# Kernel optimization log

Measured on AMD Instinct MI355X. Metric: run time of the kernel, lower is better.

Reference implementation:

```python
import jax, jax.numpy as jnp
import numpy as np
import math

D_MODEL = 512
N_HEADS = 8
D_K = D_MODEL // N_HEADS
B, N = 2, 2048


def setup_inputs() -> dict:
    key = jax.random.key(0)
    ks = jax.random.split(key, 13)
    s = 1.0 / math.sqrt(D_MODEL)
    inp = {
        "x": jax.random.normal(ks[0], (B, N, D_MODEL), dtype=jnp.float32),
        "D": jax.random.uniform(ks[1], (B, N, N), dtype=jnp.float32),
        "A": jax.random.uniform(ks[2], (B, N, N), dtype=jnp.float32),
        "Wq": jax.random.normal(ks[3], (D_MODEL, D_MODEL), dtype=jnp.float32) * s,
        "bq": jnp.zeros((D_MODEL,), dtype=jnp.float32),
        "Wk": jax.random.normal(ks[4], (D_MODEL, D_MODEL), dtype=jnp.float32) * s,
        "bk": jnp.zeros((D_MODEL,), dtype=jnp.float32),
        "Wv": jax.random.normal(ks[5], (D_MODEL, D_MODEL), dtype=jnp.float32) * s,
        "bv": jnp.zeros((D_MODEL,), dtype=jnp.float32),
        "Wo": jax.random.normal(ks[6], (D_MODEL, D_MODEL), dtype=jnp.float32) * s,
        "bo": jnp.zeros((D_MODEL,), dtype=jnp.float32),
        # learned per-head bias scalars; init nonzero so biases matter numerically
        "w_d": jax.random.normal(ks[7], (1, N_HEADS, 1, 1), dtype=jnp.float32) * 0.1,
        "w_a": jax.random.normal(ks[8], (1, N_HEADS, 1, 1), dtype=jnp.float32) * 0.1,
    }
    return inp


def reference(x, D, A, Wq, bq, Wk, bk, Wv, bv, Wo, bo, w_d, w_a):
    b, n, _ = x.shape
    # project and split heads: (B, H, N, d_k)
    def heads(W, bias):
        return (x @ W.T + bias).reshape(b, n, N_HEADS, D_K).transpose(0, 2, 1, 3)
    q = heads(Wq, bq)
    k = heads(Wk, bk)
    v = heads(Wv, bv)
    scale = 1.0 / math.sqrt(D_K)
    # (B, H, N, N) scores with learned-scalar-weighted tree biases
    scores = jnp.einsum("bhqd,bhkd->bhqk", q, k) * scale
    scores = scores + w_d * D[:, None, :, :] + w_a * A[:, None, :, :]
    attn = jax.nn.softmax(scores, axis=-1)
    out = jnp.einsum("bhqk,bhkd->bhqd", attn, v)
    out = out.transpose(0, 2, 1, 3).reshape(b, n, D_MODEL)
    return out @ Wo.T + bo
```

## Files before the change

### kernel.cpp

```cpp
#include <hip/hip_runtime.h>
#include <hip/hip_bf16.h>
#include <math.h>

typedef unsigned short ushort_t;
typedef unsigned int   uint_t;
typedef __attribute__((ext_vector_type(8))) short  bf16x8;
typedef __attribute__((ext_vector_type(4))) float  f32x4;
typedef __attribute__((ext_vector_type(4))) int    int4v;
typedef __attribute__((ext_vector_type(2))) int    i32x2;
typedef __attribute__((ext_vector_type(4))) short  s16x4;

#define MFMA16(a, b, c) __builtin_amdgcn_mfma_f32_16x16x32_bf16((a), (b), (c), 0, 0, 0)

static constexpr int BATCH = 2;
static constexpr int SEQ   = 2048;
static constexpr int DMODEL = 512;
static constexpr int NHEADS = 8;
static constexpr int DK    = 64;
static constexpr int MROWS = BATCH * SEQ;
static constexpr int XE = MROWS * DMODEL;
static constexpr int WE = DMODEL * DMODEL;
static constexpr int NQKV = 3 * DMODEL;
static constexpr int NSPLIT = 4;
static constexpr int KB_PER = (SEQ / 64) / NSPLIT;

static constexpr float QSCALE_L2E = 0.18033688011112043f;
static constexpr float L2E = 1.4426950408889634f;

__device__ __forceinline__ ushort_t f2bf(float f) {
  unsigned int u = __builtin_bit_cast(unsigned int, f);
  u = (u + 0x7FFFu + ((u >> 16) & 1u)) >> 16;
  return (ushort_t)u;
}

__device__ __forceinline__ float fexp2(float x) {
  float r;
  asm("v_exp_f32 %0, %1" : "=v"(r) : "v"(x));
  return r;
}

__device__ __forceinline__ int cvt_pk_bf16(float a, float b) {
  int r;
  asm("v_cvt_pk_bf16_f32 %0, %1, %2" : "=v"(r) : "v"(a), "v"(b));
  return r;
}

__device__ __forceinline__ float rowmax16(float x) {
  int t;
  t = __builtin_amdgcn_mov_dpp(__builtin_bit_cast(int, x), 0xB1, 0xF, 0xF, true);
  x = fmaxf(x, __builtin_bit_cast(float, t));
  t = __builtin_amdgcn_mov_dpp(__builtin_bit_cast(int, x), 0x4E, 0xF, 0xF, true);
  x = fmaxf(x, __builtin_bit_cast(float, t));
  t = __builtin_amdgcn_mov_dpp(__builtin_bit_cast(int, x), 0x141, 0xF, 0xF, true);
  x = fmaxf(x, __builtin_bit_cast(float, t));
  t = __builtin_amdgcn_mov_dpp(__builtin_bit_cast(int, x), 0x140, 0xF, 0xF, true);
  x = fmaxf(x, __builtin_bit_cast(float, t));
  return x;
}

__device__ __forceinline__ void async16(const ushort_t* g, ushort_t* l) {
  __builtin_amdgcn_global_load_lds(
      (const __attribute__((address_space(1))) unsigned int*)g,
      (__attribute__((address_space(3))) unsigned int*)l, 16, 0, 0);
}

__global__ __launch_bounds__(256) void convert_kernel(
    const float* __restrict__ x,  const float* __restrict__ wq,
    const float* __restrict__ wk, const float* __restrict__ wv,
    const float* __restrict__ wo,
    const float* __restrict__ bq, const float* __restrict__ bk,
    const float* __restrict__ bv,
    ushort_t* __restrict__ dst, float* __restrict__ bqkv) {
  const int bid = blockIdx.x;
  if (bid == (XE + 4 * WE) / 1024) {
    for (int i = threadIdx.x; i < NQKV; i += 256) {
      bqkv[i] = (i < 512) ? bq[i] * QSCALE_L2E
              : (i < 1024) ? bk[i - 512] : bv[i - 1024];
    }
    return;
  }
  int e = (bid * 256 + threadIdx.x) * 4;
  const float* src;
  int off;
  float qs = 1.0f;
  if (e < XE)                { src = x;  off = e; }
  else if (e < XE + WE)      { src = wq; off = e - XE; qs = QSCALE_L2E; }
  else if (e < XE + 2 * WE)  { src = wk; off = e - XE - WE; }
  else if (e < XE + 3 * WE)  { src = wv; off = e - XE - 2 * WE; }
  else                       { src = wo; off = e - XE - 3 * WE; }
  float4 f = *reinterpret_cast<const float4*>(&src[off]);
  s16x4 v;
  v[0] = (short)f2bf(f.x * qs); v[1] = (short)f2bf(f.y * qs);
  v[2] = (short)f2bf(f.z * qs); v[3] = (short)f2bf(f.w * qs);
  *reinterpret_cast<s16x4*>(&dst[e]) = v;
}

__global__ __launch_bounds__(256) void pack_da_kernel(
    const float* __restrict__ Dm, const float* __restrict__ Am,
    uint_t* __restrict__ out) {
  int e = (blockIdx.x * 256 + threadIdx.x) * 4;
  float4 d = *reinterpret_cast<const float4*>(&Dm[e]);
  float4 a = *reinterpret_cast<const float4*>(&Am[e]);
  int4v v;
  v[0] = (int)((uint_t)f2bf(d.x) | ((uint_t)f2bf(a.x) << 16));
  v[1] = (int)((uint_t)f2bf(d.y) | ((uint_t)f2bf(a.y) << 16));
  v[2] = (int)((uint_t)f2bf(d.z) | ((uint_t)f2bf(a.z) << 16));
  v[3] = (int)((uint_t)f2bf(d.w) | ((uint_t)f2bf(a.w) << 16));
  *reinterpret_cast<int4v*>(&out[e]) = v;
}

template <bool F32OUT>
__global__ __launch_bounds__(256) void gemm_bt(
    const ushort_t* __restrict__ A, const ushort_t* __restrict__ Bt,
    const float* __restrict__ bias, void* __restrict__ C,
    int N, int K) {
  __shared__ ushort_t As[64][64];
  __shared__ ushort_t Bs[64][64];
  const int tid  = threadIdx.x;
  const int wave = tid >> 6, lane = tid & 63;
  const int quad = lane >> 4, l15 = lane & 15;
  const int m0 = blockIdx.y * 64, n0 = blockIdx.x * 64;

  f32x4 acc[4] = {};

  const int lrow = lane >> 3, slot = lane & 7;
  const int cswz = 8 * (slot ^ lrow);
  const ushort_t* ag = A  + (size_t)(m0 + wave * 16 + lrow) * K + cswz;
  const ushort_t* bg = Bt + (size_t)(n0 + wave * 16 + lrow) * K + cswz;
  ushort_t* la0 = &As[wave * 16][0];
  ushort_t* la1 = &As[wave * 16 + 8][0];
  ushort_t* lb0 = &Bs[wave * 16][0];
  ushort_t* lb1 = &Bs[wave * 16 + 8][0];

  const int swz = l15 & 7;

  for (int k0 = 0; k0 < K; k0 += 64) {
    __syncthreads();
    async16(ag + k0, la0);
    async16(ag + k0 + 8 * (size_t)K, la1);
    async16(bg + k0, lb0);
    async16(bg + k0 + 8 * (size_t)K, lb1);
    asm volatile("s_waitcnt vmcnt(0)" ::: "memory");
    __syncthreads();
#pragma unroll
    for (int s = 0; s < 2; s++) {
      const int acol = 8 * ((s * 4 + quad) ^ swz);
      bf16x8 af = *reinterpret_cast<const bf16x8*>(&As[wave * 16 + l15][acol]);
#pragma unroll
      for (int t = 0; t < 4; t++) {
        bf16x8 bfr = *reinterpret_cast<const bf16x8*>(&Bs[t * 16 + l15][acol]);
        acc[t] = MFMA16(af, bfr, acc[t]);
      }
    }
  }

#pragma unroll
  for (int t = 0; t < 4; t++) {
    const int col = n0 + t * 16 + l15;
    const float bv = bias[col];
#pragma unroll
    for (int rr = 0; rr < 4; rr++) {
      const int row = m0 + wave * 16 + quad * 4 + rr;
      const float v = acc[t][rr] + bv;
      if (F32OUT) reinterpret_cast<float*>(C)[(size_t)row * N + col] = v;
      else        reinterpret_cast<ushort_t*>(C)[(size_t)row * N + col] = f2bf(v);
    }
  }
}

__global__ __launch_bounds__(256) void attn_kernel(
    const ushort_t* __restrict__ QKV, const uint_t* __restrict__ DA,
    const float* __restrict__ wd, const float* __restrict__ wa,
    float* __restrict__ Opart, float* __restrict__ Mp, float* __restrict__ Lp) {
  const int qb = blockIdx.x, h = blockIdx.y;
  const int b = blockIdx.z / NSPLIT, split = blockIdx.z % NSPLIT;
  const int tid = threadIdx.x;
  const int wave = tid >> 6, lane = tid & 63;
  const int quad = lane >> 4, l15 = lane & 15;
  const int q0 = qb * 64;
  const float wdh = wd[h] * L2E, wah = wa[h] * L2E;

  __shared__ ushort_t Ks[64][64];
  __shared__ ushort_t Vts[64][64];
  __shared__ __align__(16) ushort_t Ps[4][16][72];

  const int qrow = q0 + wave * 16 + l15;
  bf16x8 qf[2];
#pragma unroll
  for (int s = 0; s < 2; s++)
    qf[s] = *reinterpret_cast<const bf16x8*>(
        &QKV[(size_t)(b * SEQ + qrow) * NQKV + h * DK + s * 32 + quad * 8]);

  bf16x8 ones;
#pragma unroll
  for (int j = 0; j < 8; j++) ones[j] = (short)0x3F80;

  float m_run[4], l_run[4];
  f32x4 o[4] = {};
#pragma unroll
  for (int rr = 0; rr < 4; rr++) { m_run[rr] = -INFINITY; l_run[rr] = 0.f; }

  const int lrow = lane >> 3, slot = lane & 7;
  const ushort_t* kg = QKV + (size_t)(b * SEQ + wave * 16 + lrow) * NQKV +
                       512 + h * DK + 8 * (slot ^ lrow);
  ushort_t* lk0 = &Ks[wave * 16][0];
  ushort_t* lk1 = &Ks[wave * 16 + 8][0];

  const int u  = tid >> 3;
  const int c7 = tid & 7;
  const int sc = c7 * 8;
  const int kv = ((u & 3) << 4) | (u >> 2);
  const ushort_t* vg = QKV + (size_t)(b * SEQ + kv) * NQKV + 1024 + h * DK + sc;
  const int col0 = (u & 7) + 8 * ((u >> 3) ^ c7);
  const int col1 = (u & 7) + 8 * (((u >> 3) + 4) ^ c7);

  const int swz = l15 & 7;

  const uint_t* dap[4];
#pragma unroll
  for (int rr = 0; rr < 4; rr++)
    dap[rr] = DA + (size_t)b * SEQ * SEQ +
              (size_t)(q0 + wave * 16 + quad * 4 + rr) * SEQ + l15;

  for (int kbi = 0; kbi < KB_PER; kbi++) {
    const int k0 = (split * KB_PER + kbi) * 64;
    __syncthreads();
    async16(kg + (size_t)k0 * NQKV, lk0);
    async16(kg + (size_t)(k0 + 8) * NQKV, lk1);
    bf16x8 v0 = *reinterpret_cast<const bf16x8*>(vg + (size_t)k0 * NQKV);
    bf16x8 v1 = *reinterpret_cast<const bf16x8*>(vg + (size_t)(k0 + 8) * NQKV);
#pragma unroll
    for (int j = 0; j < 8; j++) {
      Vts[sc + j][col0] = (ushort_t)v0[j];
      Vts[sc + j][col1] = (ushort_t)v1[j];
    }
    asm volatile("s_waitcnt vmcnt(0)" ::: "memory");
    __syncthreads();

    uint_t da[4][4];
#pragma unroll
    for (int t = 0; t < 4; t++) {
#pragma unroll
      for (int rr = 0; rr < 4; rr++) da[t][rr] = dap[rr][k0 + t * 16];
    }

    f32x4 sacc[4];
#pragma unroll
    for (int t = 0; t < 4; t++) {
      bf16x8 kf0 = *reinterpret_cast<const bf16x8*>(&Ks[t * 16 + l15][8 * (quad ^ swz)]);
      bf16x8 kf1 = *reinterpret_cast<const bf16x8*>(&Ks[t * 16 + l15][8 * ((4 + quad) ^ swz)]);
      f32x4 z = {};
      z = MFMA16(qf[0], kf0, z);
      sacc[t] = MFMA16(qf[1], kf1, z);
    }

    float sv[4][4];
    float mx[4] = {-INFINITY, -INFINITY, -INFINITY, -INFINITY};
#pragma unroll
    for (int t = 0; t < 4; t++) {
#pragma unroll
      for (int rr = 0; rr < 4; rr++) {
        const float fd = __builtin_bit_cast(float, da[t][rr] << 16);
        const float fa = __builtin_bit_cast(float, da[t][rr] & 0xFFFF0000u);
        float s = fmaf(wdh, fd, fmaf(wah, fa, sacc[t][rr]));
        sv[t][rr] = s;
        mx[rr] = fmaxf(mx[rr], s);
      }
    }
#pragma unroll
    for (int rr = 0; rr < 4; rr++) mx[rr] = rowmax16(mx[rr]);

    bool grow = false;
#pragma unroll
    for (int rr = 0; rr < 4; rr++) grow |= (mx[rr] > m_run[rr] + 11.5f);
    if (__ballot(grow)) {
      float alpha[4];
#pragma unroll
      for (int rr = 0; rr < 4; rr++) {
        const float mn = fmaxf(m_run[rr], mx[rr]);
        alpha[rr] = fexp2(m_run[rr] - mn);
        m_run[rr] = mn;
        l_run[rr] *= alpha[rr];
      }
#pragma unroll
      for (int dt = 0; dt < 4; dt++)
#pragma unroll
        for (int rr = 0; rr < 4; rr++) o[dt][rr] *= alpha[rr];
    }

#pragma unroll
    for (int rr = 0; rr < 4; rr++) {
      const float m = m_run[rr];
      i32x2 w;
      w[0] = cvt_pk_bf16(fexp2(sv[0][rr] - m), fexp2(sv[1][rr] - m));
      w[1] = cvt_pk_bf16(fexp2(sv[2][rr] - m), fexp2(sv[3][rr] - m));
      *reinterpret_cast<i32x2*>(&Ps[wave][quad * 4 + rr][l15 * 4]) = w;
    }

    asm volatile("s_waitcnt lgkmcnt(0)" ::: "memory");

    f32x4 rsacc = {};
#pragma unroll
    for (int s2 = 0; s2 < 2; s2++) {
      bf16x8 pf = *reinterpret_cast<const bf16x8*>(&Ps[wave][l15][s2 * 32 + quad * 8]);
#pragma unroll
      for (int dt = 0; dt < 4; dt++) {
        const int vrow = dt * 16 + l15;
        const int vcb = (s2 * 4 + quad) ^ (vrow >> 3);
        bf16x8 vf = *reinterpret_cast<const bf16x8*>(&Vts[vrow][vcb * 8]);
        o[dt] = MFMA16(pf, vf, o[dt]);
      }
      rsacc = MFMA16(pf, ones, rsacc);
    }
#pragma unroll
    for (int rr = 0; rr < 4; rr++) l_run[rr] += rsacc[rr];
  }

  const int pidx = (((b * NHEADS + h) * 32 + qb) * NSPLIT + split);
  float* op = Opart + (size_t)pidx * 4096;
#pragma unroll
  for (int dt = 0; dt < 4; dt++) {
#pragma unroll
    for (int rr = 0; rr < 4; rr++) {
      const int row = wave * 16 + quad * 4 + rr;
      op[row * 64 + dt * 16 + l15] = o[dt][rr];
    }
  }
  if (l15 == 0) {
#pragma unroll
    for (int rr = 0; rr < 4; rr++) {
      const int row = wave * 16 + quad * 4 + rr;
      Mp[(size_t)pidx * 64 + row] = m_run[rr];
      Lp[(size_t)pidx * 64 + row] = l_run[rr];
    }
  }
}

__global__ __launch_bounds__(256) void combine_kernel(
    const float* __restrict__ Opart, const float* __restrict__ Mp,
    const float* __restrict__ Lp, ushort_t* __restrict__ AO) {
  const int qb = blockIdx.x, h = blockIdx.y, b = blockIdx.z;
  const int tid = threadIdx.x;
  const int lane = tid & 63, wq = tid >> 6;
  const int pidx0 = ((b * NHEADS + h) * 32 + qb) * NSPLIT;

  for (int r = 0; r < 16; r++) {
    const int q = wq * 16 + r;
    float m[NSPLIT], l[NSPLIT];
    float M = -INFINITY;
#pragma unroll
    for (int s = 0; s < NSPLIT; s++) {
      m[s] = Mp[(size_t)(pidx0 + s) * 64 + q];
      l[s] = Lp[(size_t)(pidx0 + s) * 64 + q];
      M = fmaxf(M, m[s]);
    }
    float L = 0.f, acc = 0.f;
#pragma unroll
    for (int s = 0; s < NSPLIT; s++) {
      const float w = fexp2(m[s] - M);
      L += l[s] * w;
      acc += Opart[(size_t)(pidx0 + s) * 4096 + q * 64 + lane] * w;
    }
    const int row = b * SEQ + qb * 64 + q;
    AO[(size_t)row * DMODEL + h * DK + lane] = f2bf(acc / L);
  }
}

extern "C" void kernel_launch(void* const* d_in, const int* in_sizes, int n_in,
                              void* d_out, int out_size, void* d_ws, size_t ws_size,
                              hipStream_t stream) {
  const float* x  = (const float*)d_in[0];
  const float* Dm = (const float*)d_in[1];
  const float* Am = (const float*)d_in[2];
  const float* Wq = (const float*)d_in[3];
  const float* bq = (const float*)d_in[4];
  const float* Wk = (const float*)d_in[5];
  const float* bk = (const float*)d_in[6];
  const float* Wv = (const float*)d_in[7];
  const float* bv = (const float*)d_in[8];
  const float* Wo = (const float*)d_in[9];
  const float* bo = (const float*)d_in[10];
  const float* wd = (const float*)d_in[11];
  const float* wa = (const float*)d_in[12];

  char* ws = (char*)d_ws;
  size_t off = 0;
  ushort_t* xb    = (ushort_t*)(ws + off); off += (size_t)XE * 2;
  ushort_t* wqkvb = (ushort_t*)(ws + off); off += (size_t)3 * WE * 2;
  ushort_t* wob   = (ushort_t*)(ws + off); off += (size_t)WE * 2;
  ushort_t* QKVb  = (ushort_t*)(ws + off); off += (size_t)MROWS * NQKV * 2;
  ushort_t* AO    = (ushort_t*)(ws + off); off += (size_t)XE * 2;
  float*    bqkv  = (float*)(ws + off);    off += (size_t)NQKV * 4;
  off = (off + 255) & ~(size_t)255;
  uint_t*   DAb   = (uint_t*)(ws + off);   off += (size_t)BATCH * SEQ * SEQ * 4;
  float*    Opart = (float*)(ws + off);    off += (size_t)512 * NSPLIT * 4096 * 4;
  float*    Mpart = (float*)(ws + off);    off += (size_t)512 * NSPLIT * 64 * 4;
  float*    Lpart = (float*)(ws + off);

  const int conv_blocks = (XE + 4 * WE) / 1024;
  convert_kernel<<<conv_blocks + 1, 256, 0, stream>>>(
      x, Wq, Wk, Wv, Wo, bq, bk, bv, xb, bqkv);
  pack_da_kernel<<<(BATCH * SEQ * SEQ) / 1024, 256, 0, stream>>>(Dm, Am, DAb);

  dim3 qkvgrid(NQKV / 64, MROWS / 64);
  gemm_bt<false><<<qkvgrid, 256, 0, stream>>>(xb, wqkvb, bqkv, QKVb, NQKV, DMODEL);

  dim3 agrid(SEQ / 64, NHEADS, BATCH * NSPLIT);
  attn_kernel<<<agrid, 256, 0, stream>>>(QKVb, DAb, wd, wa, Opart, Mpart, Lpart);
  dim3 cgrid(SEQ / 64, NHEADS, BATCH);
  combine_kernel<<<cgrid, 256, 0, stream>>>(Opart, Mpart, Lpart, AO);

  dim3 ogrid(DMODEL / 64, MROWS / 64);
  gemm_bt<true><<<ogrid, 256, 0, stream>>>(AO, wob, bo, (float*)d_out, DMODEL, DMODEL);
}
```

Baseline: 226.9 us.

## Drop D/A packing pass and use 128x128 tiles in projection GEMMs

Removes the pre-pass that packed D and A into bf16 pairs; the attention kernel now streams the fp32 D and A matrices directly, advancing per-row pointers. This removes one full read/write pass over the bias matrices and a kernel launch, but doubles the bytes attention reads per head from those matrices. The QKV and output GEMMs switch to 128x128 block tiles with a 2x2 wave layout for more register reuse, which reduces block count (notably for the output projection).

```diff
diff --git a/kernel.cpp b/kernel.cpp
--- a/kernel.cpp
+++ b/kernel.cpp
@@ -6,7 +6,6 @@
 typedef unsigned int   uint_t;
 typedef __attribute__((ext_vector_type(8))) short  bf16x8;
 typedef __attribute__((ext_vector_type(4))) float  f32x4;
-typedef __attribute__((ext_vector_type(4))) int    int4v;
 typedef __attribute__((ext_vector_type(2))) int    i32x2;
 typedef __attribute__((ext_vector_type(4))) short  s16x4;
 
@@ -95,81 +94,82 @@
   *reinterpret_cast<s16x4*>(&dst[e]) = v;
 }
 
-__global__ __launch_bounds__(256) void pack_da_kernel(
-    const float* __restrict__ Dm, const float* __restrict__ Am,
-    uint_t* __restrict__ out) {
-  int e = (blockIdx.x * 256 + threadIdx.x) * 4;
-  float4 d = *reinterpret_cast<const float4*>(&Dm[e]);
-  float4 a = *reinterpret_cast<const float4*>(&Am[e]);
-  int4v v;
-  v[0] = (int)((uint_t)f2bf(d.x) | ((uint_t)f2bf(a.x) << 16));
-  v[1] = (int)((uint_t)f2bf(d.y) | ((uint_t)f2bf(a.y) << 16));
-  v[2] = (int)((uint_t)f2bf(d.z) | ((uint_t)f2bf(a.z) << 16));
-  v[3] = (int)((uint_t)f2bf(d.w) | ((uint_t)f2bf(a.w) << 16));
-  *reinterpret_cast<int4v*>(&out[e]) = v;
-}
-
 template <bool F32OUT>
-__global__ __launch_bounds__(256) void gemm_bt(
+__global__ __launch_bounds__(256) void gemm_bt128(
     const ushort_t* __restrict__ A, const ushort_t* __restrict__ Bt,
     const float* __restrict__ bias, void* __restrict__ C,
     int N, int K) {
-  __shared__ ushort_t As[64][64];
-  __shared__ ushort_t Bs[64][64];
+  __shared__ ushort_t As[128][64];
+  __shared__ ushort_t Bs[128][64];
   const int tid  = threadIdx.x;
   const int wave = tid >> 6, lane = tid & 63;
   const int quad = lane >> 4, l15 = lane & 15;
-  const int m0 = blockIdx.y * 64, n0 = blockIdx.x * 64;
-
-  f32x4 acc[4] = {};
+  const int m0 = blockIdx.y * 128, n0 = blockIdx.x * 128;
+  const int wr = (wave >> 1) * 64, wc = (wave & 1) * 64;
+
+  f32x4 acc[4][4] = {};
 
   const int lrow = lane >> 3, slot = lane & 7;
   const int cswz = 8 * (slot ^ lrow);
-  const ushort_t* ag = A  + (size_t)(m0 + wave * 16 + lrow) * K + cswz;
-  const ushort_t* bg = Bt + (size_t)(n0 + wave * 16 + lrow) * K + cswz;
-  ushort_t* la0 = &As[wave * 16][0];
-  ushort_t* la1 = &As[wave * 16 + 8][0];
-  ushort_t* lb0 = &Bs[wave * 16][0];
-  ushort_t* lb1 = &Bs[wave * 16 + 8][0];
+  const ushort_t* ag = A  + (size_t)(m0 + wave * 8 + lrow) * K + cswz;
+  const ushort_t* bg = Bt + (size_t)(n0 + wave * 8 + lrow) * K + cswz;
+  ushort_t* la[4]; ushort_t* lb[4];
+#pragma unroll
+  for (int r0 = 0; r0 < 4; r0++) {
+    la[r0] = &As[r0 * 32 + wave * 8][0];
+    lb[r0] = &Bs[r0 * 32 + wave * 8][0];
+  }
 
   const int swz = l15 & 7;
 
   for (int k0 = 0; k0 < K; k0 += 64) {
     __syncthreads();
-    async16(ag + k0, la0);
-    async16(ag + k0 + 8 * (size_t)K, la1);
-    async16(bg + k0, lb0);
-    async16(bg + k0 + 8 * (size_t)K, lb1);
+#pragma unroll
+    for (int r0 = 0; r0 < 4; r0++)
+      async16(ag + k0 + (size_t)(r0 * 32) * K, la[r0]);
+#pragma unroll
+    for (int r0 = 0; r0 < 4; r0++)
+      async16(bg + k0 + (size_t)(r0 * 32) * K, lb[r0]);
     asm volatile("s_waitcnt vmcnt(0)" ::: "memory");
     __syncthreads();
 #pragma unroll
     for (int s = 0; s < 2; s++) {
       const int acol = 8 * ((s * 4 + quad) ^ swz);
-      bf16x8 af = *reinterpret_cast<const bf16x8*>(&As[wave * 16 + l15][acol]);
-#pragma unroll
-      for (int t = 0; t < 4; t++) {
-        bf16x8 bfr = *reinterpret_cast<const bf16x8*>(&Bs[t * 16 + l15][acol]);
-        acc[t] = MFMA16(af, bfr, acc[t]);
+      bf16x8 af[4], bfr[4];
+#pragma unroll
+      for (int i = 0; i < 4; i++)
+        af[i] = *reinterpret_cast<const bf16x8*>(&As[wr + i * 16 + l15][acol]);
+#pragma unroll
+      for (int j = 0; j < 4; j++)
+        bfr[j] = *reinterpret_cast<const bf16x8*>(&Bs[wc + j * 16 + l15][acol]);
+#pragma unroll
+      for (int i = 0; i < 4; i++)
+#pragma unroll
+        for (int j = 0; j < 4; j++)
+          acc[i][j] = MFMA16(af[i], bfr[j], acc[i][j]);
+    }
+  }
+
+#pragma unroll
+  for (int j = 0; j < 4; j++) {
+    const int col = n0 + wc + j * 16 + l15;
+    const float bv = bias[col];
+#pragma unroll
+    for (int i = 0; i < 4; i++) {
+#pragma unroll
+      for (int rr = 0; rr < 4; rr++) {
+        const int row = m0 + wr + i * 16 + quad * 4 + rr;
+        const float v = acc[i][j][rr] + bv;
+        if (F32OUT) reinterpret_cast<float*>(C)[(size_t)row * N + col] = v;
+        else        reinterpret_cast<ushort_t*>(C)[(size_t)row * N + col] = f2bf(v);
       }
     }
   }
-
-#pragma unroll
-  for (int t = 0; t < 4; t++) {
-    const int col = n0 + t * 16 + l15;
-    const float bv = bias[col];
-#pragma unroll
-    for (int rr = 0; rr < 4; rr++) {
-      const int row = m0 + wave * 16 + quad * 4 + rr;
-      const float v = acc[t][rr] + bv;
-      if (F32OUT) reinterpret_cast<float*>(C)[(size_t)row * N + col] = v;
-      else        reinterpret_cast<ushort_t*>(C)[(size_t)row * N + col] = f2bf(v);
-    }
-  }
 }
 
 __global__ __launch_bounds__(256) void attn_kernel(
-    const ushort_t* __restrict__ QKV, const uint_t* __restrict__ DA,
+    const ushort_t* __restrict__ QKV,
+    const float* __restrict__ Dm, const float* __restrict__ Am,
     const float* __restrict__ wd, const float* __restrict__ wa,
     float* __restrict__ Opart, float* __restrict__ Mp, float* __restrict__ Lp) {
   const int qb = blockIdx.x, h = blockIdx.y;
@@ -216,11 +216,15 @@
 
   const int swz = l15 & 7;
 
-  const uint_t* dap[4];
-#pragma unroll
-  for (int rr = 0; rr < 4; rr++)
-    dap[rr] = DA + (size_t)b * SEQ * SEQ +
-              (size_t)(q0 + wave * 16 + quad * 4 + rr) * SEQ + l15;
+  const float* dD[4];
+  const float* dA[4];
+#pragma unroll
+  for (int rr = 0; rr < 4; rr++) {
+    const size_t rowoff = (size_t)b * SEQ * SEQ +
+        (size_t)(q0 + wave * 16 + quad * 4 + rr) * SEQ + (size_t)split * KB_PER * 64 + l15;
+    dD[rr] = Dm + rowoff;
+    dA[rr] = Am + rowoff;
+  }
 
   for (int kbi = 0; kbi < KB_PER; kbi++) {
     const int k0 = (split * KB_PER + kbi) * 64;
@@ -237,12 +241,17 @@
     asm volatile("s_waitcnt vmcnt(0)" ::: "memory");
     __syncthreads();
 
-    uint_t da[4][4];
+    float dv[4][4], av[4][4];
 #pragma unroll
     for (int t = 0; t < 4; t++) {
 #pragma unroll
-      for (int rr = 0; rr < 4; rr++) da[t][rr] = dap[rr][k0 + t * 16];
-    }
+      for (int rr = 0; rr < 4; rr++) {
+        dv[t][rr] = dD[rr][t * 16];
+        av[t][rr] = dA[rr][t * 16];
+      }
+    }
+#pragma unroll
+    for (int rr = 0; rr < 4; rr++) { dD[rr] += 64; dA[rr] += 64; }
 
     f32x4 sacc[4];
 #pragma unroll
@@ -260,9 +269,7 @@
     for (int t = 0; t < 4; t++) {
 #pragma unroll
       for (int rr = 0; rr < 4; rr++) {
-        const float fd = __builtin_bit_cast(float, da[t][rr] << 16);
-        const float fa = __builtin_bit_cast(float, da[t][rr] & 0xFFFF0000u);
-        float s = fmaf(wdh, fd, fmaf(wah, fa, sacc[t][rr]));
+        float s = fmaf(wdh, dv[t][rr], fmaf(wah, av[t][rr], sacc[t][rr]));
         sv[t][rr] = s;
         mx[rr] = fmaxf(mx[rr], s);
       }
@@ -392,7 +399,6 @@
   ushort_t* AO    = (ushort_t*)(ws + off); off += (size_t)XE * 2;
   float*    bqkv  = (float*)(ws + off);    off += (size_t)NQKV * 4;
   off = (off + 255) & ~(size_t)255;
-  uint_t*   DAb   = (uint_t*)(ws + off);   off += (size_t)BATCH * SEQ * SEQ * 4;
   float*    Opart = (float*)(ws + off);    off += (size_t)512 * NSPLIT * 4096 * 4;
   float*    Mpart = (float*)(ws + off);    off += (size_t)512 * NSPLIT * 64 * 4;
   float*    Lpart = (float*)(ws + off);
@@ -400,16 +406,15 @@
   const int conv_blocks = (XE + 4 * WE) / 1024;
   convert_kernel<<<conv_blocks + 1, 256, 0, stream>>>(
       x, Wq, Wk, Wv, Wo, bq, bk, bv, xb, bqkv);
-  pack_da_kernel<<<(BATCH * SEQ * SEQ) / 1024, 256, 0, stream>>>(Dm, Am, DAb);
-
-  dim3 qkvgrid(NQKV / 64, MROWS / 64);
-  gemm_bt<false><<<qkvgrid, 256, 0, stream>>>(xb, wqkvb, bqkv, QKVb, NQKV, DMODEL);
+
+  dim3 qkvgrid(NQKV / 128, MROWS / 128);
+  gemm_bt128<false><<<qkvgrid, 256, 0, stream>>>(xb, wqkvb, bqkv, QKVb, NQKV, DMODEL);
 
   dim3 agrid(SEQ / 64, NHEADS, BATCH * NSPLIT);
-  attn_kernel<<<agrid, 256, 0, stream>>>(QKVb, DAb, wd, wa, Opart, Mpart, Lpart);
+  attn_kernel<<<agrid, 256, 0, stream>>>(QKVb, Dm, Am, wd, wa, Opart, Mpart, Lpart);
   dim3 cgrid(SEQ / 64, NHEADS, BATCH);
   combine_kernel<<<cgrid, 256, 0, stream>>>(Opart, Mpart, Lpart, AO);
 
-  dim3 ogrid(DMODEL / 64, MROWS / 64);
-  gemm_bt<true><<<ogrid, 256, 0, stream>>>(AO, wob, bo, (float*)d_out, DMODEL, DMODEL);
-}
+  dim3 ogrid(DMODEL / 128, MROWS / 128);
+  gemm_bt128<true><<<ogrid, 256, 0, stream>>>(AO, wob, bo, (float*)d_out, DMODEL, DMODEL);
+}
```

Measured after the change: 225.6 us. Within noise of the previous version (-0.5%).
